# Performance work log

Hardware: AMD Instinct MI355X
Metric: run time of the kernel (lower is better)

Reference implementation:

```python
import jax, jax.numpy as jnp
import numpy as np

MID = 64        # conf.mid_channels
N_INV = 6       # n_layers=8 -> range(1, n_layers-1) -> 6 involution blocks
K = 7           # involution kernel size
GROUP_CH = 16   # RedNet default group_channels
GROUPS = MID // GROUP_CH   # 4
RED = MID // 4             # reduction_ratio = 4 -> 16


def conv2d(x, w, b=None, pad=0):
    out = jax.lax.conv_general_dilated(
        x, w, window_strides=(1, 1), padding=[(pad, pad), (pad, pad)],
        dimension_numbers=('NCHW', 'OIHW', 'NCHW'))
    if b is not None:
        out = out + b[None, :, None, None]
    return out


def extract_patches(x, k):
    # x: (B,C,H,W) -> (B,C,k*k,H,W), same-padded (torch nn.Unfold with pad=k//2)
    p = k // 2
    xp = jnp.pad(x, ((0, 0), (0, 0), (p, p), (p, p)))
    H, W = x.shape[2], x.shape[3]
    slices = [xp[:, :, i:i + H, j:j + W] for i in range(k) for j in range(k)]
    return jnp.stack(slices, axis=2)


def involution(x, red_w, bn_gamma, bn_beta, span_w, span_b):
    # kernel-generation branch: 1x1 conv (no bias) -> BN(eval, mean=0,var=1) -> ReLU -> 1x1 conv
    t = conv2d(x, red_w)                                     # (B,RED,H,W)
    t = bn_gamma[None, :, None, None] * t + bn_beta[None, :, None, None]
    t = jax.nn.relu(t)
    w = conv2d(t, span_w, span_b)                            # (B,K*K*GROUPS,H,W)
    B, _, H, W = w.shape
    w = w.reshape(B, GROUPS, K * K, H, W)
    patches = extract_patches(x, K).reshape(B, GROUPS, GROUP_CH, K * K, H, W)
    out = jnp.einsum('bgkhw,bgckhw->bgchw', w, patches)      # per-pixel dynamic conv
    return out.reshape(B, MID, H, W)


def setup_inputs() -> dict:
    key = jax.random.key(0)
    ks = jax.random.split(key, 12)
    s = 0.05
    inp = {
        'input_tensor': jax.random.normal(ks[0], (1, 3, 128, 128), jnp.float32),
        'conv_in_w': jax.random.normal(ks[1], (MID, 3, 3, 3), jnp.float32) * s,
        'conv_in_b': jax.random.normal(ks[2], (MID,), jnp.float32) * s,
        'red_w': jax.random.normal(ks[3], (N_INV, RED, MID, 1, 1), jnp.float32) * s,
        'bn_gamma': jnp.ones((N_INV, RED), jnp.float32),
        'bn_beta': jnp.zeros((N_INV, RED), jnp.float32),
        'span_w': jax.random.normal(ks[4], (N_INV, K * K * GROUPS, RED, 1, 1), jnp.float32) * s,
        'span_b': jax.random.normal(ks[5], (N_INV, K * K * GROUPS), jnp.float32) * s,
        'conv_out_w': jax.random.normal(ks[6], (12, MID, 3, 3), jnp.float32) * s,
        'conv_out_b': jax.random.normal(ks[7], (12,), jnp.float32) * s,
    }
    return inp


def reference(input_tensor, conv_in_w, conv_in_b, red_w, bn_gamma, bn_beta,
              span_w, span_b, conv_out_w, conv_out_b):
    x = conv2d(input_tensor, conv_in_w, conv_in_b, pad=2)     # (B,MID,H+2,W+2)
    for l in range(N_INV):
        x = jax.nn.relu(involution(x, red_w[l], bn_gamma[l], bn_beta[l],
                                   span_w[l], span_b[l]))
    pixel = conv2d(x, conv_out_w, conv_out_b, pad=0)          # (B,12,H,W)
    # PixelShuffle(2): (B,12,H,W) -> (B,3,2H,2W)
    B, _, H, W = pixel.shape
    out = pixel.reshape(B, 3, 2, 2, H, W).transpose(0, 1, 4, 2, 5, 3)
    return out.reshape(B, 3, 2 * H, 2 * W)
```

## Files before the change

kernel.cpp:

```cpp
#include <hip/hip_runtime.h>


#define HH 130
#define SP 136
#define PPL (SP*SP)
#define GP (PPL*16)
#define XBUF2 (4*GP)
#define OFF_TF (2*XBUF2)

__global__ __launch_bounds__(256) void conv_in_kernel(
        const float* __restrict__ inf, const float* __restrict__ W,
        const float* __restrict__ b, float* __restrict__ x0,
        float* __restrict__ x1) {
    const int tid = threadIdx.x;
    if (blockIdx.x >= 67) {
        int idx = ((blockIdx.x - 67)*4 + blockIdx.y)*256 + tid;
        if (idx < 3192) {
            int bsel = idx & 1, e = idx >> 1;
            int r, c;
            if (e < 816) { r = e/136; c = e%136; if (r >= 3) r += 130; }
            else { int j = e-816; r = 3 + j/6; int m = j%6; c = (m<3)? m : m+130; }
            float* base = (bsel ? x1 : x0) + ((size_t)r*SP + c)*16;
            float4 z = make_float4(0.f,0.f,0.f,0.f);
            #pragma unroll
            for (int g2 = 0; g2 < 4; ++g2)
                #pragma unroll
                for (int q = 0; q < 4; ++q)
                    *(float4*)(base + (size_t)g2*GP + q*4) = z;
        }
        return;
    }
    __shared__ float wl[448];
    const int g = blockIdx.y;
    for (int i = tid; i < 448; i += 256)
        wl[i] = (i < 432) ? W[g*432 + i] : b[g*16 + (i-432)];
    __syncthreads();
    int px = blockIdx.x*256 + tid;
    int pxc = px < 16900 ? px : 16899;
    int h = pxc/130, w = pxc%130;
    float xv[27];
    #pragma unroll
    for (int i = 0; i < 3; ++i)
      #pragma unroll
      for (int ky = 0; ky < 3; ++ky) {
        int y = h - 2 + ky;
        #pragma unroll
        for (int kx = 0; kx < 3; ++kx) {
            int xx = w - 2 + kx;
            float v = 0.f;
            if ((unsigned)y < 128u && (unsigned)xx < 128u)
                v = inf[i*16384 + y*128 + xx];
            xv[i*9 + ky*3 + kx] = v;
        }
      }
    float acc[16];
    #pragma unroll
    for (int c = 0; c < 16; ++c) {
        float a = wl[432 + c];
        #pragma unroll
        for (int t = 0; t < 27; ++t) a += wl[c*27 + t] * xv[t];
        acc[c] = a;
    }
    if (px < 16900) {
        float* dst = x0 + (size_t)g*GP + ((size_t)(h+3)*SP + (w+3))*16;
        #pragma unroll
        for (int q = 0; q < 4; ++q)
            *(float4*)(dst + q*4) =
                make_float4(acc[q*4], acc[q*4+1], acc[q*4+2], acc[q*4+3]);
    }
}

__global__ __launch_bounds__(256) void t_kernel(
        const float* __restrict__ x, float* __restrict__ tf,
        const float* __restrict__ redw,
        const float* __restrict__ gamma, const float* __restrict__ beta)
{
    const int wid = blockIdx.x;
    const int T = (wid & 7)*37 + (wid >> 3);
    if (T >= 289) return;
    const int ty = (T/17)*8, tx = (T%17)*8;
    const int tid = threadIdx.x;
    const int lane = tid & 63;
    const int rq = __builtin_amdgcn_readfirstlane(tid >> 6);
    const int h = ty + (lane >> 3), w = tx + (lane & 7);
    const int hc = h < HH ? h : HH-1, wc = w < HH ? w : HH-1;

    const float* xb = x + ((size_t)(hc+3)*SP + (wc+3))*16;
    const float* rw = redw + rq*4*64;
    float a0=0.f, a1=0.f, a2=0.f, a3=0.f;
    #pragma unroll
    for (int g2 = 0; g2 < 4; ++g2) {
        #pragma unroll
        for (int q = 0; q < 4; ++q) {
            float4 v = *(const float4*)(xb + (size_t)g2*GP + q*4);
            int c = g2*16 + q*4;
            a0 += rw[c]*v.x     + rw[c+1]*v.y   + rw[c+2]*v.z   + rw[c+3]*v.w;
            a1 += rw[64+c]*v.x  + rw[65+c]*v.y  + rw[66+c]*v.z  + rw[67+c]*v.w;
            a2 += rw[128+c]*v.x + rw[129+c]*v.y + rw[130+c]*v.z + rw[131+c]*v.w;
            a3 += rw[192+c]*v.x + rw[193+c]*v.y + rw[194+c]*v.z + rw[195+c]*v.w;
        }
    }
    if (h < HH && w < HH) {
        int r0 = rq*4;
        float4 t4;
        t4.x = fmaxf(gamma[r0+0]*a0 + beta[r0+0], 0.f);
        t4.y = fmaxf(gamma[r0+1]*a1 + beta[r0+1], 0.f);
        t4.z = fmaxf(gamma[r0+2]*a2 + beta[r0+2], 0.f);
        t4.w = fmaxf(gamma[r0+3]*a3 + beta[r0+3], 0.f);
        *(float4*)(tf + ((size_t)h*HH + w)*16 + r0) = t4;
    }
}

__global__ __launch_bounds__(256, 4) void e_kernel(
        const float* __restrict__ x, const float* __restrict__ tf,
        const float* __restrict__ spanw,
        const float* __restrict__ spanb,
        float* __restrict__ xout)
{
    __shared__ float xl[4][14][17][4];
    __shared__ float wl[49][68];
    const int wid = blockIdx.x;
    const int slot = wid >> 3;
    const int T = (wid & 7)*37 + (slot >> 2);
    if (T >= 289) return;
    const int g = slot & 3;
    const int ty = (T/17)*8, tx = (T%17)*8;
    const int tid = threadIdx.x;
    const int px = tid & 63;
    const int wv = __builtin_amdgcn_readfirstlane(tid >> 6);
    const int sr = px >> 3, sc = px & 7;

    for (int i = tid; i < 784; i += 256) {
        int q = i & 3, p = i >> 2;
        int r = p / 14, c = p % 14;
        int gr = ty + r, gc = tx + c;
        gr = gr < SP ? gr : SP-1;
        gc = gc < SP ? gc : SP-1;
        float4 v = *(const float4*)(x + (size_t)g*GP
                                    + ((size_t)gr*SP + gc)*16 + q*4);
        *(float4*)&xl[q][r][c][0] = v;
    }

    {
        const int hh = min(ty + sr, HH-1), ww = min(tx + sc, HH-1);
        const float* tp = tf + ((size_t)hh*HH + ww)*16;
        float t16[16];
        #pragma unroll
        for (int q = 0; q < 4; ++q) {
            float4 v = *(const float4*)(tp + q*4);
            t16[q*4]=v.x; t16[q*4+1]=v.y; t16[q*4+2]=v.z; t16[q*4+3]=v.w;
        }
        const float* sw = spanw + g*784;
        const float* sb = spanb + g*49;
        const int k0 = wv ? (wv*12 + 1) : 0;
        #pragma unroll
        for (int j = 0; j < 12; ++j) {
            int k = k0 + j;
            float a = sb[k];
            #pragma unroll
            for (int r = 0; r < 16; ++r) a += sw[k*16 + r] * t16[r];
            wl[k][px] = a;
        }
        if (wv == 0) {
            float a = sb[12];
            #pragma unroll
            for (int r = 0; r < 16; ++r) a += sw[12*16 + r] * t16[r];
            wl[12][px] = a;
        }
    }
    __syncthreads();

    const int cq = wv;
    float4 acc = make_float4(0.f, 0.f, 0.f, 0.f);
    #pragma unroll
    for (int i = 0; i < 7; ++i)
        #pragma unroll
        for (int j = 0; j < 7; ++j) {
            float4 xv = *(const float4*)&xl[cq][sr + i][sc + j][0];
            float wk = wl[i*7 + j][px];
            acc.x += wk*xv.x; acc.y += wk*xv.y;
            acc.z += wk*xv.z; acc.w += wk*xv.w;
        }

    const int h = ty + sr, w = tx + sc;
    if (h < HH && w < HH) {
        float4 o;
        o.x = fmaxf(acc.x, 0.f); o.y = fmaxf(acc.y, 0.f);
        o.z = fmaxf(acc.z, 0.f); o.w = fmaxf(acc.w, 0.f);
        *(float4*)(xout + (size_t)g*GP
                   + ((size_t)(h+3)*SP + (w+3))*16 + cq*4) = o;
    }
}

__global__ __launch_bounds__(256) void conv_out_ps_kernel(
        const float* __restrict__ x, const float* __restrict__ W,
        const float* __restrict__ b, float* __restrict__ out)
{
    __shared__ float xh[64*120];
    __shared__ float wl[6912];
    const int tid = threadIdx.x;
    const int ty = blockIdx.y*8, tx = blockIdx.x*8;

    for (int idx = tid; idx < 6912; idx += 256) wl[idx] = W[idx];
    for (int idx = tid; idx < 1600; idx += 256) {
        int g = idx/400, rem = idx%400;
        int p100 = rem>>2, q = rem&3;
        int r = p100/10, cl = p100%10;
        float4 v = *(const float4*)(x + (size_t)g*GP
                     + ((size_t)(ty + r + 3)*SP + tx + cl + 3)*16 + q*4);
        int c0 = g*16 + q*4;
        xh[(c0+0)*120 + r*12 + cl] = v.x;
        xh[(c0+1)*120 + r*12 + cl] = v.y;
        xh[(c0+2)*120 + r*12 + cl] = v.z;
        xh[(c0+3)*120 + r*12 + cl] = v.w;
    }
    __syncthreads();

    const int wave = __builtin_amdgcn_readfirstlane(tid >> 6);
    const int lane = tid & 63;
    const int s = lane >> 2, cq = lane & 3;
    const int sr = s >> 1, pc0 = (s & 1)*4;
    float acc[3][4] = {};

    for (int c = cq*16; c < cq*16 + 16; ++c) {
        #pragma unroll
        for (int ky = 0; ky < 3; ++ky) {
            const float* xb = &xh[c*120 + (sr + ky)*12 + pc0];
            float4 xa = *(const float4*)xb;
            float2 xm = *(const float2*)(xb + 4);
            float xr[6] = {xa.x, xa.y, xa.z, xa.w, xm.x, xm.y};
            #pragma unroll
            for (int oj = 0; oj < 3; ++oj) {
                const float* wp = &wl[((wave*3 + oj)*64 + c)*9 + ky*3];
                #pragma unroll
                for (int kx = 0; kx < 3; ++kx) {
                    float wv = wp[kx];
                    #pragma unroll
                    for (int q = 0; q < 4; ++q)
                        acc[oj][q] += wv * xr[kx + q];
                }
            }
        }
    }

    #pragma unroll
    for (int oj = 0; oj < 3; ++oj)
        #pragma unroll
        for (int q = 0; q < 4; ++q) {
            float v = acc[oj][q];
            v += __shfl_xor(v, 1, 64);
            v += __shfl_xor(v, 2, 64);
            acc[oj][q] = v;
        }

    if (cq == 0) {
        #pragma unroll
        for (int oj = 0; oj < 3; ++oj) {
            int o = wave*3 + oj;
            float bo = b[o];
            int c3 = o >> 2, r = (o >> 1) & 1, s2 = o & 1;
            int h = ty + sr;
            #pragma unroll
            for (int q = 0; q < 4; ++q) {
                int w = tx + pc0 + q;
                out[c3*65536 + (2*h + r)*256 + 2*w + s2] = acc[oj][q] + bo;
            }
        }
    }
}

extern "C" void kernel_launch(void* const* d_in, const int* in_sizes, int n_in,
                              void* d_out, int out_size, void* d_ws, size_t ws_size,
                              hipStream_t stream) {
    const float* inf   = (const float*)d_in[0];
    const float* cinw  = (const float*)d_in[1];
    const float* cinb  = (const float*)d_in[2];
    const float* redw  = (const float*)d_in[3];
    const float* gam   = (const float*)d_in[4];
    const float* bet   = (const float*)d_in[5];
    const float* spw   = (const float*)d_in[6];
    const float* spb   = (const float*)d_in[7];
    const float* cow   = (const float*)d_in[8];
    const float* cob   = (const float*)d_in[9];

    float* ws = (float*)d_ws;
    float* x0 = ws;
    float* x1 = ws + XBUF2;
    float* tfield = ws + OFF_TF;

    conv_in_kernel<<<dim3(80, 4), 256, 0, stream>>>(inf, cinw, cinb, x0, x1);

    float* cur = x0; float* nxt = x1;
    for (int l = 0; l < 6; ++l) {
        t_kernel<<<296, 256, 0, stream>>>(
            cur, tfield, redw + l*1024, gam + l*16, bet + l*16);
        e_kernel<<<1184, 256, 0, stream>>>(
            cur, tfield, spw + l*3136, spb + l*196, nxt);
        float* t = cur; cur = nxt; nxt = t;
    }

    conv_out_ps_kernel<<<dim3(16, 16), 256, 0, stream>>>(
        cur, cow, cob, (float*)d_out);
}
```

Measured before the change: 212.6 us.

## Fuse next layer's reduction conv into involution kernel via atomics

Removes the per-layer t_kernel launch by having each e_kernel compute the next layer's 1x1 reduction projection from its output, accumulating partial sums across the four channel groups with LDS atomics and then global atomics into a rotating triple-buffered t-field. BN and ReLU move into the consumer e_kernel, and a separate t0 kernel handles the first layer. This cuts five launches and the re-read of x, but adds global float atomics, buffer zeroing, and an extra barrier in the e_kernel. Float atomic ordering also makes the summation order nondeterministic.

Result: slower. 330.2 us (+55.3%).

```diff
diff --git a/kernel.cpp b/kernel.cpp
--- a/kernel.cpp
+++ b/kernel.cpp
@@ -6,7 +6,10 @@
 #define PPL (SP*SP)
 #define GP (PPL*16)
 #define XBUF2 (4*GP)
-#define OFF_TF (2*XBUF2)
+#define TFSZ (16900*16)
+#define OFF_T0 (2*XBUF2)
+#define OFF_T1 (OFF_T0 + TFSZ)
+#define OFF_T2 (OFF_T1 + TFSZ)
 
 __global__ __launch_bounds__(256) void conv_in_kernel(
         const float* __restrict__ inf, const float* __restrict__ W,
@@ -70,16 +73,25 @@
     }
 }
 
-__global__ __launch_bounds__(256) void t_kernel(
-        const float* __restrict__ x, float* __restrict__ tf,
-        const float* __restrict__ redw,
-        const float* __restrict__ gamma, const float* __restrict__ beta)
+__global__ __launch_bounds__(256) void t0_kernel(
+        const float* __restrict__ x, float* __restrict__ tb0,
+        float* __restrict__ tb1,
+        const float* __restrict__ redw)
 {
     const int wid = blockIdx.x;
     const int T = (wid & 7)*37 + (wid >> 3);
     if (T >= 289) return;
     const int ty = (T/17)*8, tx = (T%17)*8;
     const int tid = threadIdx.x;
+
+    {
+        int zr = tid >> 5, zc4 = tid & 31;
+        int zh = ty + zr, zw = tx + (zc4 >> 2);
+        if (zh < HH && zw < HH)
+            *(float4*)(tb1 + ((size_t)zh*HH + zw)*16 + (zc4 & 3)*4) =
+                make_float4(0.f,0.f,0.f,0.f);
+    }
+
     const int lane = tid & 63;
     const int rq = __builtin_amdgcn_readfirstlane(tid >> 6);
     const int h = ty + (lane >> 3), w = tx + (lane & 7);
@@ -102,23 +114,26 @@
     }
     if (h < HH && w < HH) {
         int r0 = rq*4;
-        float4 t4;
-        t4.x = fmaxf(gamma[r0+0]*a0 + beta[r0+0], 0.f);
-        t4.y = fmaxf(gamma[r0+1]*a1 + beta[r0+1], 0.f);
-        t4.z = fmaxf(gamma[r0+2]*a2 + beta[r0+2], 0.f);
-        t4.w = fmaxf(gamma[r0+3]*a3 + beta[r0+3], 0.f);
-        *(float4*)(tf + ((size_t)h*HH + w)*16 + r0) = t4;
+        *(float4*)(tb0 + ((size_t)h*HH + w)*16 + r0) =
+            make_float4(a0, a1, a2, a3);
     }
 }
 
 __global__ __launch_bounds__(256, 4) void e_kernel(
-        const float* __restrict__ x, const float* __restrict__ tf,
+        const float* __restrict__ x,
+        const float* __restrict__ tread,
+        float* __restrict__ tacc,
+        float* __restrict__ tzero,
+        const float* __restrict__ gamma, const float* __restrict__ beta,
         const float* __restrict__ spanw,
         const float* __restrict__ spanb,
-        float* __restrict__ xout)
+        const float* __restrict__ redwn,
+        float* __restrict__ xout,
+        const int doNext)
 {
     __shared__ float xl[4][14][17][4];
     __shared__ float wl[49][68];
+    __shared__ float sl[64][16];
     const int wid = blockIdx.x;
     const int slot = wid >> 3;
     const int T = (wid & 7)*37 + (slot >> 2);
@@ -140,15 +155,26 @@
                                     + ((size_t)gr*SP + gc)*16 + q*4);
         *(float4*)&xl[q][r][c][0] = v;
     }
+    if (doNext) {
+        *(float4*)&sl[tid >> 2][(tid & 3)*4] = make_float4(0.f,0.f,0.f,0.f);
+        int zr = tid >> 5, zc4 = tid & 31;
+        int zh = ty + zr, zw = tx + (zc4 >> 2);
+        if (zh < HH && zw < HH)
+            *(float4*)(tzero + ((size_t)zh*HH + zw)*16 + (zc4 & 3)*4) =
+                make_float4(0.f,0.f,0.f,0.f);
+    }
 
     {
         const int hh = min(ty + sr, HH-1), ww = min(tx + sc, HH-1);
-        const float* tp = tf + ((size_t)hh*HH + ww)*16;
+        const float* tp = tread + ((size_t)hh*HH + ww)*16;
         float t16[16];
         #pragma unroll
         for (int q = 0; q < 4; ++q) {
             float4 v = *(const float4*)(tp + q*4);
-            t16[q*4]=v.x; t16[q*4+1]=v.y; t16[q*4+2]=v.z; t16[q*4+3]=v.w;
+            t16[q*4+0] = fmaxf(gamma[q*4+0]*v.x + beta[q*4+0], 0.f);
+            t16[q*4+1] = fmaxf(gamma[q*4+1]*v.y + beta[q*4+1], 0.f);
+            t16[q*4+2] = fmaxf(gamma[q*4+2]*v.z + beta[q*4+2], 0.f);
+            t16[q*4+3] = fmaxf(gamma[q*4+3]*v.w + beta[q*4+3], 0.f);
         }
         const float* sw = spanw + g*784;
         const float* sb = spanb + g*49;
@@ -182,13 +208,34 @@
             acc.z += wk*xv.z; acc.w += wk*xv.w;
         }
 
-    const int h = ty + sr, w = tx + sc;
-    if (h < HH && w < HH) {
-        float4 o;
-        o.x = fmaxf(acc.x, 0.f); o.y = fmaxf(acc.y, 0.f);
-        o.z = fmaxf(acc.z, 0.f); o.w = fmaxf(acc.w, 0.f);
+    const int h = ty + sr, ww2 = tx + sc;
+    const bool valid = (h < HH) && (ww2 < HH);
+    float4 o = make_float4(fmaxf(acc.x,0.f), fmaxf(acc.y,0.f),
+                           fmaxf(acc.z,0.f), fmaxf(acc.w,0.f));
+    if (valid)
         *(float4*)(xout + (size_t)g*GP
-                   + ((size_t)(h+3)*SP + (w+3))*16 + cq*4) = o;
+                   + ((size_t)(h+3)*SP + (ww2+3))*16 + cq*4) = o;
+
+    if (doNext) {
+        if (valid) {
+            const int c0 = g*16 + cq*4;
+            #pragma unroll
+            for (int r = 0; r < 16; ++r) {
+                float p = redwn[r*64 + c0]*o.x + redwn[r*64 + c0+1]*o.y
+                        + redwn[r*64 + c0+2]*o.z + redwn[r*64 + c0+3]*o.w;
+                atomicAdd(&sl[px][r], p);
+            }
+        }
+        __syncthreads();
+        int px2 = tid >> 2, r0 = (tid & 3)*4;
+        int h2 = ty + (px2 >> 3), w2 = tx + (px2 & 7);
+        if (h2 < HH && w2 < HH) {
+            float* dt = tacc + ((size_t)h2*HH + w2)*16 + r0;
+            atomicAdd(dt+0, sl[px2][r0+0]);
+            atomicAdd(dt+1, sl[px2][r0+1]);
+            atomicAdd(dt+2, sl[px2][r0+2]);
+            atomicAdd(dt+3, sl[px2][r0+3]);
+        }
     }
 }
 
@@ -286,16 +333,21 @@
     float* ws = (float*)d_ws;
     float* x0 = ws;
     float* x1 = ws + XBUF2;
-    float* tfield = ws + OFF_TF;
+    float* tb[3] = { ws + OFF_T0, ws + OFF_T1, ws + OFF_T2 };
 
     conv_in_kernel<<<dim3(80, 4), 256, 0, stream>>>(inf, cinw, cinb, x0, x1);
+
+    t0_kernel<<<296, 256, 0, stream>>>(x0, tb[0], tb[1], redw);
 
     float* cur = x0; float* nxt = x1;
     for (int l = 0; l < 6; ++l) {
-        t_kernel<<<296, 256, 0, stream>>>(
-            cur, tfield, redw + l*1024, gam + l*16, bet + l*16);
+        const int doNext = (l < 5);
         e_kernel<<<1184, 256, 0, stream>>>(
-            cur, tfield, spw + l*3136, spb + l*196, nxt);
+            cur, tb[l % 3], tb[(l+1) % 3], tb[(l+2) % 3],
+            gam + l*16, bet + l*16,
+            spw + l*3136, spb + l*196,
+            redw + (doNext ? (l+1)*1024 : 0),
+            nxt, doNext);
         float* t = cur; cur = nxt; nxt = t;
     }
 
```
